# Kernel optimization log

Hardware: AMD Instinct MI355X
Metric: run time of the kernel (lower is better)

## Reference

```python
import jax, jax.numpy as jnp
import numpy as np

B, LC, LQ, D = 16, 2048, 1024, 512


def setup_inputs() -> dict:
    key = jax.random.key(0)
    k1, k2, k3 = jax.random.split(key, 3)
    context = jax.random.normal(k1, (B, LC, D), dtype=jnp.float32)
    query = jax.random.normal(k2, (LQ, D), dtype=jnp.float32)
    # nn.Linear(3*D, 1, bias=False).weight  -> [1, 3D]
    w = jax.random.normal(k3, (1, 3 * D), dtype=jnp.float32) * (1.0 / np.sqrt(3 * D))
    return {"context": context, "query": query, "w": w}


def reference(context, query, w):
    # context: [B, Lc, D], query: [Lq, D], w: [1, 3D]
    d = context.shape[-1]
    wc, wq, wm = w[0, :d], w[0, d:2 * d], w[0, 2 * d:]
    # S[b,i,j] = <context[b,i], wc> + <query[j], wq> + <context[b,i]*wm, query[j]>
    # (algebraic collapse of Linear(cat(c, q, c*q)) -- identical math, no 4D tensor)
    S = ((context @ wc)[:, :, None]
         + (query @ wq)[None, None, :]
         + jnp.einsum('bid,jd->bij', context * wm, query))  # [B, Lc, Lq]
    # softmax over context dim (dim=1), then permute -> A[b,j,i]
    A = jnp.transpose(jax.nn.softmax(S, axis=1), (0, 2, 1))  # [B, Lq, Lc]
    # query mask: sign(|sum_d query|), same for every batch element
    qmask = jnp.sign(jnp.abs(jnp.sum(query, axis=-1)))  # [Lq]
    A = A * qmask[None, :, None]
    # attd[b,j,i,d] = A[b,j,i] * context[b,i,d]
    # G_att[b,i,d] = context[b,i,d] * sum_j A[b,j,i]
    colsum = jnp.sum(A, axis=1)  # [B, Lc]
    G_att = context * colsum[:, :, None]  # [B, Lc, D]
    # H[b,j,d] = sum_i A[b,j,i] * context[b,i,d]
    H = jnp.einsum('bji,bid->bjd', A, context)  # [B, Lq, D]
    G = jnp.concatenate((context, G_att), axis=2)  # [B, Lc, 2D]
    return (G, H)
```

## Files before the change

kernel.cpp:

```cpp
#include <hip/hip_runtime.h>
#include <stdint.h>

#define BB 16
#define LC 2048
#define LQ 1024
#define DD 512

typedef _Float16 f16x8 __attribute__((ext_vector_type(8)));
typedef _Float16 f16x4 __attribute__((ext_vector_type(4)));
typedef float f32x4 __attribute__((ext_vector_type(4)));

#define MFMA16 __builtin_amdgcn_mfma_f32_16x16x32_f16

__device__ __forceinline__ void async16(_Float16* lds, const _Float16* g) {
    __builtin_amdgcn_global_load_lds(
        (const __attribute__((address_space(1))) void*)g,
        (__attribute__((address_space(3))) void*)lds, 16, 0, 0);
}

__global__ void zero_k(float* __restrict__ p, int n) {
    int i = blockIdx.x * blockDim.x + threadIdx.x;
    if (i < n) p[i] = 0.0f;
}

__global__ __launch_bounds__(256) void prep_ctx(
    const float* __restrict__ ctx, const float* __restrict__ w,
    _Float16* __restrict__ cm, _Float16* __restrict__ ct, float* __restrict__ cb)
{
    __shared__ _Float16 sm[64][68];
    const int b = blockIdx.z;
    const int i0 = blockIdx.y * 64;
    const int d0 = blockIdx.x * 64;
    const int t = threadIdx.x;
    const int tx = t & 15, ty = t >> 4;
    const float* wc = w;
    const float* wm = w + 2 * DD;
    const float4 wc4 = *(const float4*)(wc + d0 + tx * 4);
    const float4 wm4 = *(const float4*)(wm + d0 + tx * 4);
    for (int k = 0; k < 4; ++k) {
        const int r = ty + 16 * k;
        const int ig = i0 + r;
        const float4 v = *(const float4*)(ctx + ((size_t)(b * LC + ig)) * DD + d0 + tx * 4);
        f16x4 cmv = { (_Float16)(v.x * wm4.x), (_Float16)(v.y * wm4.y),
                      (_Float16)(v.z * wm4.z), (_Float16)(v.w * wm4.w) };
        *(f16x4*)(cm + ((size_t)(b * LC + ig)) * DD + d0 + tx * 4) = cmv;
        sm[tx * 4 + 0][r] = (_Float16)v.x;
        sm[tx * 4 + 1][r] = (_Float16)v.y;
        sm[tx * 4 + 2][r] = (_Float16)v.z;
        sm[tx * 4 + 3][r] = (_Float16)v.w;
        float p = v.x * wc4.x + v.y * wc4.y + v.z * wc4.z + v.w * wc4.w;
        p += __shfl_xor(p, 1); p += __shfl_xor(p, 2);
        p += __shfl_xor(p, 4); p += __shfl_xor(p, 8);
        if (tx == 0) atomicAdd(&cb[b * LC + ig], p);
    }
    __syncthreads();
    for (int k = 0; k < 4; ++k) {
        const int dd = ty + 16 * k;
        f16x4 o = *(const f16x4*)(&sm[dd][tx * 4]);
        *(f16x4*)(ct + ((size_t)(b * DD + d0 + dd)) * LC + i0 + tx * 4) = o;
    }
}

__global__ __launch_bounds__(128) void prep_q(
    const float* __restrict__ q, const float* __restrict__ w,
    _Float16* __restrict__ qh, float* __restrict__ qb, float* __restrict__ qmask)
{
    const int j = blockIdx.x;
    const int t = threadIdx.x;
    const float* wq = w + DD;
    const float4 v = *(const float4*)(q + (size_t)j * DD + t * 4);
    const float4 wq4 = *(const float4*)(wq + t * 4);
    f16x4 qv = { (_Float16)v.x, (_Float16)v.y, (_Float16)v.z, (_Float16)v.w };
    *(f16x4*)(qh + (size_t)j * DD + t * 4) = qv;
    float dq = v.x * wq4.x + v.y * wq4.y + v.z * wq4.z + v.w * wq4.w;
    float sq = v.x + v.y + v.z + v.w;
    for (int m = 1; m < 64; m <<= 1) { dq += __shfl_xor(dq, m); sq += __shfl_xor(sq, m); }
    __shared__ float sd[2], ss[2];
    if ((t & 63) == 0) { sd[t >> 6] = dq; ss[t >> 6] = sq; }
    __syncthreads();
    if (t == 0) {
        qb[j] = sd[0] + sd[1];
        float s = ss[0] + ss[1];
        qmask[j] = (s != 0.0f) ? 1.0f : 0.0f;
    }
}

__global__ __launch_bounds__(256) void gemm1(
    const _Float16* __restrict__ qh, const _Float16* __restrict__ cm,
    const float* __restrict__ cb, const float* __restrict__ qb,
    _Float16* __restrict__ E, float* __restrict__ lsum)
{
    __shared__ __align__(16) _Float16 smA[128 * 32];
    __shared__ __align__(16) _Float16 smB[128 * 32];
    const int b = blockIdx.z;
    const int m0 = blockIdx.x * 128;
    const int n0 = blockIdx.y * 128;
    const int t = threadIdx.x;
    const int lane = t & 63;
    const int wid = t >> 6;
    const int wvm = wid >> 1, wvn = wid & 1;
    const int li = lane & 15, lg = lane >> 4;
    f32x4 acc[4][4] = {};
    const int srow = lane >> 2;
    const int scol = (lane & 3) * 8;
    const _Float16* gA0 = qh + (size_t)(m0 + wid * 32 + srow) * DD + scol;
    const _Float16* gA1 = gA0 + (size_t)16 * DD;
    const _Float16* gB0 = cm + ((size_t)(b * LC + n0 + wid * 32 + srow)) * DD + scol;
    const _Float16* gB1 = gB0 + (size_t)16 * DD;
    _Float16* sA0 = smA + wid * 32 * 32;
    _Float16* sA1 = sA0 + 16 * 32;
    _Float16* sB0 = smB + wid * 32 * 32;
    _Float16* sB1 = sB0 + 16 * 32;
    for (int ks = 0; ks < DD; ks += 32) {
        __syncthreads();
        async16(sA0, gA0 + ks);
        async16(sA1, gA1 + ks);
        async16(sB0, gB0 + ks);
        async16(sB1, gB1 + ks);
        __syncthreads();
        f16x8 af[4], bf[4];
        #pragma unroll
        for (int mt = 0; mt < 4; ++mt)
            af[mt] = *(const f16x8*)(smA + (wvm * 64 + mt * 16 + li) * 32 + lg * 8);
        #pragma unroll
        for (int nt = 0; nt < 4; ++nt)
            bf[nt] = *(const f16x8*)(smB + (wvn * 64 + nt * 16 + li) * 32 + lg * 8);
        #pragma unroll
        for (int mt = 0; mt < 4; ++mt)
            #pragma unroll
            for (int nt = 0; nt < 4; ++nt)
                acc[mt][nt] = MFMA16(af[mt], bf[nt], acc[mt][nt], 0, 0, 0);
    }
    __syncthreads();
    float* rs = (float*)smA;
    if (t < 128) rs[t] = 0.0f;
    __syncthreads();
    float cbv[4];
    #pragma unroll
    for (int nt = 0; nt < 4; ++nt) cbv[nt] = cb[b * LC + n0 + wvn * 64 + nt * 16 + li];
    #pragma unroll
    for (int mt = 0; mt < 4; ++mt) {
        #pragma unroll
        for (int r = 0; r < 4; ++r) {
            const int jl = wvm * 64 + mt * 16 + lg * 4 + r;
            const int j = m0 + jl;
            const float qbv = qb[j];
            _Float16* Erow = E + ((size_t)(b * LQ + j)) * LC + n0 + wvn * 64;
            float rsv = 0.0f;
            #pragma unroll
            for (int nt = 0; nt < 4; ++nt) {
                float e = __expf(acc[mt][nt][r] + cbv[nt] + qbv);
                rsv += e;
                Erow[nt * 16 + li] = (_Float16)e;
            }
            rsv += __shfl_xor(rsv, 1); rsv += __shfl_xor(rsv, 2);
            rsv += __shfl_xor(rsv, 4); rsv += __shfl_xor(rsv, 8);
            if (li == 0) atomicAdd(&rs[jl], rsv);
        }
    }
    __syncthreads();
    if (t < 128) atomicAdd(&lsum[b * LQ + m0 + t], rs[t]);
}

__global__ __launch_bounds__(256) void gemm2(
    const _Float16* __restrict__ E, const _Float16* __restrict__ ct,
    const float* __restrict__ lsum, const float* __restrict__ qmask,
    float* __restrict__ H)
{
    __shared__ __align__(16) _Float16 smA[128 * 32];
    __shared__ __align__(16) _Float16 smB[128 * 32];
    const int b = blockIdx.z;
    const int m0 = blockIdx.x * 128;
    const int n0 = blockIdx.y * 128;
    const int t = threadIdx.x;
    const int lane = t & 63;
    const int wid = t >> 6;
    const int wvm = wid >> 1, wvn = wid & 1;
    const int li = lane & 15, lg = lane >> 4;
    f32x4 acc[4][4] = {};
    const int srow = lane >> 2;
    const int scol = (lane & 3) * 8;
    const _Float16* gA0 = E + ((size_t)(b * LQ + m0 + wid * 32 + srow)) * LC + scol;
    const _Float16* gA1 = gA0 + (size_t)16 * LC;
    const _Float16* gB0 = ct + ((size_t)(b * DD + n0 + wid * 32 + srow)) * LC + scol;
    const _Float16* gB1 = gB0 + (size_t)16 * LC;
    _Float16* sA0 = smA + wid * 32 * 32;
    _Float16* sA1 = sA0 + 16 * 32;
    _Float16* sB0 = smB + wid * 32 * 32;
    _Float16* sB1 = sB0 + 16 * 32;
    for (int ks = 0; ks < LC; ks += 32) {
        __syncthreads();
        async16(sA0, gA0 + ks);
        async16(sA1, gA1 + ks);
        async16(sB0, gB0 + ks);
        async16(sB1, gB1 + ks);
        __syncthreads();
        f16x8 af[4], bf[4];
        #pragma unroll
        for (int mt = 0; mt < 4; ++mt)
            af[mt] = *(const f16x8*)(smA + (wvm * 64 + mt * 16 + li) * 32 + lg * 8);
        #pragma unroll
        for (int nt = 0; nt < 4; ++nt)
            bf[nt] = *(const f16x8*)(smB + (wvn * 64 + nt * 16 + li) * 32 + lg * 8);
        #pragma unroll
        for (int mt = 0; mt < 4; ++mt)
            #pragma unroll
            for (int nt = 0; nt < 4; ++nt)
                acc[mt][nt] = MFMA16(af[mt], bf[nt], acc[mt][nt], 0, 0, 0);
    }
    #pragma unroll
    for (int mt = 0; mt < 4; ++mt) {
        #pragma unroll
        for (int r = 0; r < 4; ++r) {
            const int j = m0 + wvm * 64 + mt * 16 + lg * 4 + r;
            const float s = qmask[j] / lsum[b * LQ + j];
            float* Hrow = H + ((size_t)(b * LQ + j)) * DD + n0 + wvn * 64;
            #pragma unroll
            for (int nt = 0; nt < 4; ++nt)
                Hrow[nt * 16 + li] = acc[mt][nt][r] * s;
        }
    }
}

__global__ __launch_bounds__(256) void colsum_k(
    const _Float16* __restrict__ E, const float* __restrict__ lsum,
    const float* __restrict__ qmask, float* __restrict__ cs)
{
    __shared__ float ssm[64];
    const int b = blockIdx.y;
    const int j0 = blockIdx.x * 64;
    const int t = threadIdx.x;
    if (t < 64) {
        const int jj = j0 + t;
        ssm[t] = qmask[jj] / lsum[b * LQ + jj];
    }
    __syncthreads();
    const _Float16* Eb = E + ((size_t)(b * LQ + j0)) * LC + t * 8;
    float acc[8] = {};
    #pragma unroll 4
    for (int j = 0; j < 64; ++j) {
        f16x8 v = *(const f16x8*)(Eb + (size_t)j * LC);
        const float s = ssm[j];
        #pragma unroll
        for (int q = 0; q < 8; ++q) acc[q] += s * (float)v[q];
    }
    float* base = cs + b * LC + t * 8;
    #pragma unroll
    for (int q = 0; q < 8; ++q) atomicAdd(base + q, acc[q]);
}

__global__ __launch_bounds__(128) void gwrite(
    const float* __restrict__ ctx, const float* __restrict__ cs, float* __restrict__ G)
{
    const int b = blockIdx.y, i = blockIdx.x, t = threadIdx.x;
    const float c = cs[b * LC + i];
    const size_t ro = (size_t)(b * LC + i);
    const float4 v = *(const float4*)(ctx + ro * DD + t * 4);
    float4 u; u.x = v.x * c; u.y = v.y * c; u.z = v.z * c; u.w = v.w * c;
    *(float4*)(G + ro * (2 * DD) + t * 4) = v;
    *(float4*)(G + ro * (2 * DD) + DD + t * 4) = u;
}

extern "C" void kernel_launch(void* const* d_in, const int* in_sizes, int n_in,
                              void* d_out, int out_size, void* d_ws, size_t ws_size,
                              hipStream_t stream)
{
    (void)in_sizes; (void)n_in; (void)out_size; (void)ws_size;
    const float* ctx = (const float*)d_in[0];
    const float* qry = (const float*)d_in[1];
    const float* w   = (const float*)d_in[2];
    float* G = (float*)d_out;
    float* H = G + (size_t)BB * LC * (2 * DD);

    char* ws = (char*)d_ws;
    _Float16* E  = (_Float16*)ws;
    _Float16* cm = (_Float16*)(ws + ((size_t)64 << 20));
    _Float16* ct = (_Float16*)(ws + ((size_t)96 << 20));
    _Float16* qh = (_Float16*)(ws + ((size_t)128 << 20));
    float* stats = (float*)(ws + ((size_t)130 << 20));
    float* cb    = stats;
    float* lsum  = cb + BB * LC;
    float* cs    = lsum + BB * LQ;
    float* qb    = cs + BB * LC;
    float* qmask = qb + LQ;

    const int nzero = BB * LC + BB * LQ + BB * LC;
    zero_k<<<dim3((nzero + 255) / 256), 256, 0, stream>>>(stats, nzero);
    prep_ctx<<<dim3(DD / 64, LC / 64, BB), 256, 0, stream>>>(ctx, w, cm, ct, cb);
    prep_q<<<dim3(LQ), 128, 0, stream>>>(qry, w, qh, qb, qmask);
    gemm1<<<dim3(LQ / 128, LC / 128, BB), 256, 0, stream>>>(qh, cm, cb, qb, E, lsum);
    gemm2<<<dim3(LQ / 128, DD / 128, BB), 256, 0, stream>>>(E, ct, lsum, qmask, H);
    colsum_k<<<dim3(LQ / 64, BB), 256, 0, stream>>>(E, lsum, qmask, cs);
    gwrite<<<dim3(LC, BB), 128, 0, stream>>>(ctx, cs, G);
}
```

Measured before the change: 391.5 us.

## Double-buffer GEMM loads, split-K gemm2 with atomics, and fuse prep_ctx over D

Both GEMMs now double-buffer their LDS tiles, so the next K slice is fetched asynchronously while the current one is computed, and one barrier per iteration is removed. gemm2 is split four ways along the context dimension to give more blocks, and partial H sums are accumulated with float atomics into an H zeroed beforehand. The zero kernel now also clears H. prep_ctx loops over all D chunks within one block, so cb is written directly instead of built up with atomics. The costs are extra atomic traffic and the H zeroing pass, and gemm2's LDS use doubles.

```diff
diff --git a/kernel.cpp b/kernel.cpp
--- a/kernel.cpp
+++ b/kernel.cpp
@@ -18,9 +18,10 @@
         (__attribute__((address_space(3))) void*)lds, 16, 0, 0);
 }
 
-__global__ void zero_k(float* __restrict__ p, int n) {
-    int i = blockIdx.x * blockDim.x + threadIdx.x;
-    if (i < n) p[i] = 0.0f;
+__global__ __launch_bounds__(256) void zero_k(float* __restrict__ H, float* __restrict__ stats) {
+    const int i = blockIdx.x * 256 + threadIdx.x;
+    if (i < (BB * LQ * DD) / 4) ((float4*)H)[i] = make_float4(0.f, 0.f, 0.f, 0.f);
+    if (i < BB * LQ + BB * LC) stats[i] = 0.0f;
 }
 
 __global__ __launch_bounds__(256) void prep_ctx(
@@ -28,36 +29,42 @@
     _Float16* __restrict__ cm, _Float16* __restrict__ ct, float* __restrict__ cb)
 {
     __shared__ _Float16 sm[64][68];
-    const int b = blockIdx.z;
-    const int i0 = blockIdx.y * 64;
-    const int d0 = blockIdx.x * 64;
+    const int b = blockIdx.y;
+    const int i0 = blockIdx.x * 64;
     const int t = threadIdx.x;
     const int tx = t & 15, ty = t >> 4;
-    const float* wc = w;
-    const float* wm = w + 2 * DD;
-    const float4 wc4 = *(const float4*)(wc + d0 + tx * 4);
-    const float4 wm4 = *(const float4*)(wm + d0 + tx * 4);
+    float cbacc[4] = {0.f, 0.f, 0.f, 0.f};
+    for (int dc = 0; dc < 8; ++dc) {
+        const int d0 = dc * 64;
+        const float4 wc4 = *(const float4*)(w + d0 + tx * 4);
+        const float4 wm4 = *(const float4*)(w + 2 * DD + d0 + tx * 4);
+        if (dc) __syncthreads();
+        for (int k = 0; k < 4; ++k) {
+            const int r = ty + 16 * k;
+            const int ig = i0 + r;
+            const float4 v = *(const float4*)(ctx + ((size_t)(b * LC + ig)) * DD + d0 + tx * 4);
+            f16x4 cmv = { (_Float16)(v.x * wm4.x), (_Float16)(v.y * wm4.y),
+                          (_Float16)(v.z * wm4.z), (_Float16)(v.w * wm4.w) };
+            *(f16x4*)(cm + ((size_t)(b * LC + ig)) * DD + d0 + tx * 4) = cmv;
+            sm[tx * 4 + 0][r] = (_Float16)v.x;
+            sm[tx * 4 + 1][r] = (_Float16)v.y;
+            sm[tx * 4 + 2][r] = (_Float16)v.z;
+            sm[tx * 4 + 3][r] = (_Float16)v.w;
+            cbacc[k] += v.x * wc4.x + v.y * wc4.y + v.z * wc4.z + v.w * wc4.w;
+        }
+        __syncthreads();
+        for (int k = 0; k < 4; ++k) {
+            const int dd = ty + 16 * k;
+            f16x4 o = *(const f16x4*)(&sm[dd][tx * 4]);
+            *(f16x4*)(ct + ((size_t)(b * DD + d0 + dd)) * LC + i0 + tx * 4) = o;
+        }
+    }
+    #pragma unroll
     for (int k = 0; k < 4; ++k) {
-        const int r = ty + 16 * k;
-        const int ig = i0 + r;
-        const float4 v = *(const float4*)(ctx + ((size_t)(b * LC + ig)) * DD + d0 + tx * 4);
-        f16x4 cmv = { (_Float16)(v.x * wm4.x), (_Float16)(v.y * wm4.y),
-                      (_Float16)(v.z * wm4.z), (_Float16)(v.w * wm4.w) };
-        *(f16x4*)(cm + ((size_t)(b * LC + ig)) * DD + d0 + tx * 4) = cmv;
-        sm[tx * 4 + 0][r] = (_Float16)v.x;
-        sm[tx * 4 + 1][r] = (_Float16)v.y;
-        sm[tx * 4 + 2][r] = (_Float16)v.z;
-        sm[tx * 4 + 3][r] = (_Float16)v.w;
-        float p = v.x * wc4.x + v.y * wc4.y + v.z * wc4.z + v.w * wc4.w;
+        float p = cbacc[k];
         p += __shfl_xor(p, 1); p += __shfl_xor(p, 2);
         p += __shfl_xor(p, 4); p += __shfl_xor(p, 8);
-        if (tx == 0) atomicAdd(&cb[b * LC + ig], p);
-    }
-    __syncthreads();
-    for (int k = 0; k < 4; ++k) {
-        const int dd = ty + 16 * k;
-        f16x4 o = *(const f16x4*)(&sm[dd][tx * 4]);
-        *(f16x4*)(ct + ((size_t)(b * DD + d0 + dd)) * LC + i0 + tx * 4) = o;
+        if (tx == 0) cb[b * LC + i0 + ty + 16 * k] = p;
     }
 }
 
@@ -90,8 +97,8 @@
     const float* __restrict__ cb, const float* __restrict__ qb,
     _Float16* __restrict__ E, float* __restrict__ lsum)
 {
-    __shared__ __align__(16) _Float16 smA[128 * 32];
-    __shared__ __align__(16) _Float16 smB[128 * 32];
+    __shared__ __align__(16) _Float16 smA[2][128 * 32];
+    __shared__ __align__(16) _Float16 smB[2][128 * 32];
     const int b = blockIdx.z;
     const int m0 = blockIdx.x * 128;
     const int n0 = blockIdx.y * 128;
@@ -103,28 +110,33 @@
     f32x4 acc[4][4] = {};
     const int srow = lane >> 2;
     const int scol = (lane & 3) * 8;
+    const int soff = wid * 32 * 32;
     const _Float16* gA0 = qh + (size_t)(m0 + wid * 32 + srow) * DD + scol;
     const _Float16* gA1 = gA0 + (size_t)16 * DD;
     const _Float16* gB0 = cm + ((size_t)(b * LC + n0 + wid * 32 + srow)) * DD + scol;
     const _Float16* gB1 = gB0 + (size_t)16 * DD;
-    _Float16* sA0 = smA + wid * 32 * 32;
-    _Float16* sA1 = sA0 + 16 * 32;
-    _Float16* sB0 = smB + wid * 32 * 32;
-    _Float16* sB1 = sB0 + 16 * 32;
-    for (int ks = 0; ks < DD; ks += 32) {
+    async16(&smA[0][soff], gA0);
+    async16(&smA[0][soff + 512], gA1);
+    async16(&smB[0][soff], gB0);
+    async16(&smB[0][soff + 512], gB1);
+    #pragma unroll
+    for (int it = 0; it < 16; ++it) {
+        const int p = it & 1;
         __syncthreads();
-        async16(sA0, gA0 + ks);
-        async16(sA1, gA1 + ks);
-        async16(sB0, gB0 + ks);
-        async16(sB1, gB1 + ks);
-        __syncthreads();
+        if (it + 1 < 16) {
+            const int ks = (it + 1) * 32;
+            async16(&smA[p ^ 1][soff], gA0 + ks);
+            async16(&smA[p ^ 1][soff + 512], gA1 + ks);
+            async16(&smB[p ^ 1][soff], gB0 + ks);
+            async16(&smB[p ^ 1][soff + 512], gB1 + ks);
+        }
         f16x8 af[4], bf[4];
         #pragma unroll
         for (int mt = 0; mt < 4; ++mt)
-            af[mt] = *(const f16x8*)(smA + (wvm * 64 + mt * 16 + li) * 32 + lg * 8);
+            af[mt] = *(const f16x8*)(&smA[p][(wvm * 64 + mt * 16 + li) * 32 + lg * 8]);
         #pragma unroll
         for (int nt = 0; nt < 4; ++nt)
-            bf[nt] = *(const f16x8*)(smB + (wvn * 64 + nt * 16 + li) * 32 + lg * 8);
+            bf[nt] = *(const f16x8*)(&smB[p][(wvn * 64 + nt * 16 + li) * 32 + lg * 8]);
         #pragma unroll
         for (int mt = 0; mt < 4; ++mt)
             #pragma unroll
@@ -167,9 +179,10 @@
     const float* __restrict__ lsum, const float* __restrict__ qmask,
     float* __restrict__ H)
 {
-    __shared__ __align__(16) _Float16 smA[128 * 32];
-    __shared__ __align__(16) _Float16 smB[128 * 32];
-    const int b = blockIdx.z;
+    __shared__ __align__(16) _Float16 smA[2][128 * 32];
+    __shared__ __align__(16) _Float16 smB[2][128 * 32];
+    const int kc = blockIdx.z & 3;
+    const int b  = blockIdx.z >> 2;
     const int m0 = blockIdx.x * 128;
     const int n0 = blockIdx.y * 128;
     const int t = threadIdx.x;
@@ -180,28 +193,33 @@
     f32x4 acc[4][4] = {};
     const int srow = lane >> 2;
     const int scol = (lane & 3) * 8;
-    const _Float16* gA0 = E + ((size_t)(b * LQ + m0 + wid * 32 + srow)) * LC + scol;
+    const int soff = wid * 32 * 32;
+    const _Float16* gA0 = E + ((size_t)(b * LQ + m0 + wid * 32 + srow)) * LC + kc * 512 + scol;
     const _Float16* gA1 = gA0 + (size_t)16 * LC;
-    const _Float16* gB0 = ct + ((size_t)(b * DD + n0 + wid * 32 + srow)) * LC + scol;
+    const _Float16* gB0 = ct + ((size_t)(b * DD + n0 + wid * 32 + srow)) * LC + kc * 512 + scol;
     const _Float16* gB1 = gB0 + (size_t)16 * LC;
-    _Float16* sA0 = smA + wid * 32 * 32;
-    _Float16* sA1 = sA0 + 16 * 32;
-    _Float16* sB0 = smB + wid * 32 * 32;
-    _Float16* sB1 = sB0 + 16 * 32;
-    for (int ks = 0; ks < LC; ks += 32) {
+    async16(&smA[0][soff], gA0);
+    async16(&smA[0][soff + 512], gA1);
+    async16(&smB[0][soff], gB0);
+    async16(&smB[0][soff + 512], gB1);
+    #pragma unroll
+    for (int it = 0; it < 16; ++it) {
+        const int p = it & 1;
         __syncthreads();
-        async16(sA0, gA0 + ks);
-        async16(sA1, gA1 + ks);
-        async16(sB0, gB0 + ks);
-        async16(sB1, gB1 + ks);
-        __syncthreads();
+        if (it + 1 < 16) {
+            const int ks = (it + 1) * 32;
+            async16(&smA[p ^ 1][soff], gA0 + ks);
+            async16(&smA[p ^ 1][soff + 512], gA1 + ks);
+            async16(&smB[p ^ 1][soff], gB0 + ks);
+            async16(&smB[p ^ 1][soff + 512], gB1 + ks);
+        }
         f16x8 af[4], bf[4];
         #pragma unroll
         for (int mt = 0; mt < 4; ++mt)
-            af[mt] = *(const f16x8*)(smA + (wvm * 64 + mt * 16 + li) * 32 + lg * 8);
+            af[mt] = *(const f16x8*)(&smA[p][(wvm * 64 + mt * 16 + li) * 32 + lg * 8]);
         #pragma unroll
         for (int nt = 0; nt < 4; ++nt)
-            bf[nt] = *(const f16x8*)(smB + (wvn * 64 + nt * 16 + li) * 32 + lg * 8);
+            bf[nt] = *(const f16x8*)(&smB[p][(wvn * 64 + nt * 16 + li) * 32 + lg * 8]);
         #pragma unroll
         for (int mt = 0; mt < 4; ++mt)
             #pragma unroll
@@ -217,7 +235,7 @@
             float* Hrow = H + ((size_t)(b * LQ + j)) * DD + n0 + wvn * 64;
             #pragma unroll
             for (int nt = 0; nt < 4; ++nt)
-                Hrow[nt * 16 + li] = acc[mt][nt][r] * s;
+                atomicAdd(Hrow + nt * 16 + li, acc[mt][nt][r] * s);
         }
     }
 }
@@ -284,12 +302,11 @@
     float* qb    = cs + BB * LC;
     float* qmask = qb + LQ;
 
-    const int nzero = BB * LC + BB * LQ + BB * LC;
-    zero_k<<<dim3((nzero + 255) / 256), 256, 0, stream>>>(stats, nzero);
-    prep_ctx<<<dim3(DD / 64, LC / 64, BB), 256, 0, stream>>>(ctx, w, cm, ct, cb);
+    zero_k<<<dim3((BB * LQ * DD / 4 + 255) / 256), 256, 0, stream>>>(H, lsum);
+    prep_ctx<<<dim3(LC / 64, BB), 256, 0, stream>>>(ctx, w, cm, ct, cb);
     prep_q<<<dim3(LQ), 128, 0, stream>>>(qry, w, qh, qb, qmask);
     gemm1<<<dim3(LQ / 128, LC / 128, BB), 256, 0, stream>>>(qh, cm, cb, qb, E, lsum);
-    gemm2<<<dim3(LQ / 128, DD / 128, BB), 256, 0, stream>>>(E, ct, lsum, qmask, H);
+    gemm2<<<dim3(LQ / 128, DD / 128, BB * 4), 256, 0, stream>>>(E, ct, lsum, qmask, H);
     colsum_k<<<dim3(LQ / 64, BB), 256, 0, stream>>>(E, lsum, qmask, cs);
     gwrite<<<dim3(LC, BB), 128, 0, stream>>>(ctx, cs, G);
 }
```

Result: slower. 466.8 us (+19.2%).
